# Optimization experiments

Measured on AMD Instinct MI355X. Metric: run time of the kernel, lower is better.

The kernel has to match this reference:

```python
import jax, jax.numpy as jnp
import numpy as np

MAX_LEN = 30
CONST_VAL = 0.0

def setup_inputs() -> dict:
    key = jax.random.key(0)
    k1, k2, k3 = jax.random.split(key, 3)
    B, T, F = 131072, 30, 10
    inputs = jax.random.normal(k1, (B, T, F), dtype=jnp.float32)
    w1 = jax.random.normal(k2, (1, MAX_LEN), dtype=jnp.float32) * 0.05
    w2 = jax.random.normal(k3, (1, MAX_LEN), dtype=jnp.float32) * 0.05
    return {"inputs": inputs, "w1": w1, "w2": w2}

def reference(inputs, w1, w2):
    B, T, F = inputs.shape  # T == 30 (hardcoded split count), F < MAX_LEN
    # matmul of (B,1,1) scalar with (1,max_len) == outer product -> (B, max_len)
    r1 = inputs[:, 0, 0][:, None] * w1[0]  # (B, 30)
    r2 = inputs[:, 0, 1][:, None] * w2[0]  # (B, 30)
    # concat along last dim then flatten rows, matching tf concat+reshape(-1,2)
    rc = jnp.stack([r1, r2], axis=-1).reshape(-1, 2)  # (N, 2), N = B*30
    N = rc.shape[0]
    K = (MAX_LEN - F) // 2  # number of shifted copies (original + K-1 shifts)
    # pad K-1 constant rows on top; shift i is rows [K-1-i : K-1-i+N] of padded
    pad = jnp.full((K - 1, 2), CONST_VAL, dtype=jnp.float32)
    P = jnp.concatenate([pad, rc], axis=0)  # (N+K-1, 2)
    shifts = jnp.stack(
        [jax.lax.dynamic_slice_in_dim(P, K - 1 - i, N, axis=0) for i in range(K)],
        axis=1,
    )  # (N, K, 2); shift-major column order matches tf.concat axis=1 order
    tens = shifts.reshape(N, 2 * K)  # (N, 2K)
    # tf.split(30, axis=0) + stack(axis=1): piece j row a = tens[j*B + a]
    tens = tens.reshape(30, B, 2 * K).transpose(1, 0, 2)  # (B, 30, 2K)
    return jnp.concatenate([tens, inputs[:, :, 2:]], axis=2)  # (B, 30, 2K+F-2)
```

## Files before the change

kernel.cpp:

```cpp
#include <hip/hip_runtime.h>


typedef float f32x4 __attribute__((ext_vector_type(4)));
typedef float f32x2 __attribute__((ext_vector_type(2)));

__global__ __launch_bounds__(256) void pack_kernel(const float* __restrict__ inp,
                                                   float2* __restrict__ xc, int B) {
    int q = blockIdx.x * blockDim.x + threadIdx.x;
    if (q < B) {
        const float* p = inp + (size_t)q * 300;
        xc[q] = make_float2(p[0], p[1]);
    }
}

__global__ __launch_bounds__(256) void main_kernel(
    const float* __restrict__ inp,
    const float2* __restrict__ xc,
    const float* __restrict__ w1,
    const float* __restrict__ w2,
    float* __restrict__ out,
    int B, int nrows) {
    __shared__ float w1s[30], w2s[30];
    int t = threadIdx.x;
    if (t < 30) w1s[t] = w1[t];
    else if (t >= 32 && t < 62) w2s[t - 32] = w2[t - 32];
    __syncthreads();

    int pairid = t >> 1;
    int h = t & 1;
    int row = blockIdx.x * 128 + pairid;
    if (row >= nrows) return;

    int b = row / 30;
    int j = row - b * 30;
    int m0 = j * B + b;
    int q0 = m0 / 30;
    int r0 = m0 - q0 * 30;

    float2 xa = xc[q0];
    float2 xb = (q0 >= 1) ? xc[q0 - 1] : make_float2(0.f, 0.f);

    float* orow = out + (size_t)row * 28;

    if (h == 0) {
        float f[14];
#pragma unroll
        for (int k = 0; k < 14; ++k) {
            int i = k >> 1, c = k & 1;
            bool useA = (r0 >= i);
            int r = useA ? (r0 - i) : (r0 - i + 30);
            float x = c ? (useA ? xa.y : xb.y) : (useA ? xa.x : xb.x);
            float w = c ? w2s[r] : w1s[r];
            f[k] = (m0 - i >= 0) ? x * w : 0.f;
        }
        *(f32x4*)(orow + 0)  = (f32x4){f[0], f[1], f[2], f[3]};
        *(f32x4*)(orow + 4)  = (f32x4){f[4], f[5], f[6], f[7]};
        *(f32x4*)(orow + 8)  = (f32x4){f[8], f[9], f[10], f[11]};
        *(f32x2*)(orow + 12) = (f32x2){f[12], f[13]};
    } else {
        const float* irow = inp + (size_t)row * 10;
        f32x2 a0 = *(const f32x2*)(irow + 2);
        f32x2 a1 = *(const f32x2*)(irow + 4);
        f32x2 a2 = *(const f32x2*)(irow + 6);
        f32x2 a3 = *(const f32x2*)(irow + 8);

        float f[6];
#pragma unroll
        for (int k = 14; k < 20; ++k) {
            int i = k >> 1, c = k & 1;
            bool useA = (r0 >= i);
            int r = useA ? (r0 - i) : (r0 - i + 30);
            float x = c ? (useA ? xa.y : xb.y) : (useA ? xa.x : xb.x);
            float w = c ? w2s[r] : w1s[r];
            f[k - 14] = (m0 - i >= 0) ? x * w : 0.f;
        }
        *(f32x2*)(orow + 14) = (f32x2){f[0], f[1]};
        *(f32x4*)(orow + 16) = (f32x4){f[2], f[3], f[4], f[5]};
        *(f32x4*)(orow + 20) = (f32x4){a0.x, a0.y, a1.x, a1.y};
        *(f32x4*)(orow + 24) = (f32x4){a2.x, a2.y, a3.x, a3.y};
    }
}

extern "C" void kernel_launch(void* const* d_in, const int* in_sizes, int n_in,
                              void* d_out, int out_size, void* d_ws, size_t ws_size,
                              hipStream_t stream) {
    const float* inp = (const float*)d_in[0];
    const float* w1  = (const float*)d_in[1];
    const float* w2  = (const float*)d_in[2];
    float* out = (float*)d_out;

    int B = in_sizes[0] / 300;
    int nrows = B * 30;

    float2* xc = (float2*)d_ws;

    pack_kernel<<<(B + 255) / 256, 256, 0, stream>>>(inp, xc, B);

    int grid = (nrows + 127) / 128;
    main_kernel<<<grid, 256, 0, stream>>>(inp, xc, w1, w2, out, B, nrows);
}
```

Baseline: 628.8 us.

## Assign one float4 output chunk per thread for fully coalesced stores

Changes the work split so each thread produces exactly one 16-byte chunk of the 28-float output row (7 chunks per row), instead of two threads sharing a row with uneven vector stores. Consecutive threads now write consecutive float4s, which makes stores contiguous across the wavefront. The cost is redundant index math and duplicate xc gathers per chunk, plus more threads and divisions by 7.

```diff
diff --git a/kernel.cpp b/kernel.cpp
--- a/kernel.cpp
+++ b/kernel.cpp
@@ -19,66 +19,44 @@
     const float* __restrict__ w1,
     const float* __restrict__ w2,
     float* __restrict__ out,
-    int B, int nrows) {
+    int B, int nG) {
     __shared__ float w1s[30], w2s[30];
     int t = threadIdx.x;
     if (t < 30) w1s[t] = w1[t];
     else if (t >= 32 && t < 62) w2s[t - 32] = w2[t - 32];
     __syncthreads();
 
-    int pairid = t >> 1;
-    int h = t & 1;
-    int row = blockIdx.x * 128 + pairid;
-    if (row >= nrows) return;
+    int g = blockIdx.x * 256 + t;
+    if (g >= nG) return;
+    int row = g / 7;
+    int c4 = g - row * 7;
 
-    int b = row / 30;
-    int j = row - b * 30;
-    int m0 = j * B + b;
-    int q0 = m0 / 30;
-    int r0 = m0 - q0 * 30;
-
-    float2 xa = xc[q0];
-    float2 xb = (q0 >= 1) ? xc[q0 - 1] : make_float2(0.f, 0.f);
-
-    float* orow = out + (size_t)row * 28;
-
-    if (h == 0) {
-        float f[14];
+    f32x4 v;
+    if (c4 < 5) {
+        int b = row / 30;
+        int j = row - b * 30;
+        int m0 = j * B + b;
+        int q0 = m0 / 30;
+        int r0 = m0 - q0 * 30;
+        float2 xa = xc[q0];
+        float2 xb = (q0 >= 1) ? xc[q0 - 1] : make_float2(0.f, 0.f);
 #pragma unroll
-        for (int k = 0; k < 14; ++k) {
+        for (int e = 0; e < 4; ++e) {
+            int k = c4 * 4 + e;
             int i = k >> 1, c = k & 1;
             bool useA = (r0 >= i);
             int r = useA ? (r0 - i) : (r0 - i + 30);
             float x = c ? (useA ? xa.y : xb.y) : (useA ? xa.x : xb.x);
             float w = c ? w2s[r] : w1s[r];
-            f[k] = (m0 - i >= 0) ? x * w : 0.f;
+            v[e] = (m0 - i >= 0) ? x * w : 0.f;
         }
-        *(f32x4*)(orow + 0)  = (f32x4){f[0], f[1], f[2], f[3]};
-        *(f32x4*)(orow + 4)  = (f32x4){f[4], f[5], f[6], f[7]};
-        *(f32x4*)(orow + 8)  = (f32x4){f[8], f[9], f[10], f[11]};
-        *(f32x2*)(orow + 12) = (f32x2){f[12], f[13]};
     } else {
-        const float* irow = inp + (size_t)row * 10;
-        f32x2 a0 = *(const f32x2*)(irow + 2);
-        f32x2 a1 = *(const f32x2*)(irow + 4);
-        f32x2 a2 = *(const f32x2*)(irow + 6);
-        f32x2 a3 = *(const f32x2*)(irow + 8);
-
-        float f[6];
-#pragma unroll
-        for (int k = 14; k < 20; ++k) {
-            int i = k >> 1, c = k & 1;
-            bool useA = (r0 >= i);
-            int r = useA ? (r0 - i) : (r0 - i + 30);
-            float x = c ? (useA ? xa.y : xb.y) : (useA ? xa.x : xb.x);
-            float w = c ? w2s[r] : w1s[r];
-            f[k - 14] = (m0 - i >= 0) ? x * w : 0.f;
-        }
-        *(f32x2*)(orow + 14) = (f32x2){f[0], f[1]};
-        *(f32x4*)(orow + 16) = (f32x4){f[2], f[3], f[4], f[5]};
-        *(f32x4*)(orow + 20) = (f32x4){a0.x, a0.y, a1.x, a1.y};
-        *(f32x4*)(orow + 24) = (f32x4){a2.x, a2.y, a3.x, a3.y};
+        const float* irow = inp + (size_t)row * 10 + 2 + (c4 - 5) * 4;
+        f32x2 lo = *(const f32x2*)(irow);
+        f32x2 hi = *(const f32x2*)(irow + 2);
+        v = (f32x4){lo.x, lo.y, hi.x, hi.y};
     }
+    *(f32x4*)(out + (size_t)g * 4) = v;
 }
 
 extern "C" void kernel_launch(void* const* d_in, const int* in_sizes, int n_in,
@@ -91,11 +69,12 @@
 
     int B = in_sizes[0] / 300;
     int nrows = B * 30;
+    int nG = nrows * 7;
 
     float2* xc = (float2*)d_ws;
 
     pack_kernel<<<(B + 255) / 256, 256, 0, stream>>>(inp, xc, B);
 
-    int grid = (nrows + 127) / 128;
-    main_kernel<<<grid, 256, 0, stream>>>(inp, xc, w1, w2, out, B, nrows);
+    int grid = (nG + 255) / 256;
+    main_kernel<<<grid, 256, 0, stream>>>(inp, xc, w1, w2, out, B, nG);
 }
```

Result: faster. 602.9 us (-4.1%).
